# Kernel tuning notes

Hardware: AMD Instinct MI355X
Metric: run time of the kernel (lower is better)

The kernel has to match this reference:

```python
import jax, jax.numpy as jnp
import numpy as np

T_STEPS = 16
A = 64
B = 64
N = 16          # read_N
C = 3           # channels
H = 1024        # enc_size
IN = N * N * C  # LSTM input size = 768
EPS = 1e-8


def setup_inputs() -> dict:
    key = jax.random.key(0)
    ks = jax.random.split(key, 12)
    s = 0.02
    x = jax.random.normal(ks[0], (1024, C, B, A), dtype=jnp.float32)
    W_att = jax.random.normal(ks[1], (5, H), dtype=jnp.float32) * s
    b_att = jnp.zeros((5,), dtype=jnp.float32)
    W_ih = jax.random.normal(ks[2], (4 * H, IN), dtype=jnp.float32) * s
    W_hh = jax.random.normal(ks[3], (4 * H, H), dtype=jnp.float32) * s
    b_ih = jnp.zeros((4 * H,), dtype=jnp.float32)
    b_hh = jnp.zeros((4 * H,), dtype=jnp.float32)
    W_fc0 = jax.random.normal(ks[4], (H, H), dtype=jnp.float32) * s
    b_fc0 = jnp.zeros((H,), dtype=jnp.float32)
    W_fc = jax.random.normal(ks[5], (10, H), dtype=jnp.float32) * s
    b_fc = jnp.zeros((10,), dtype=jnp.float32)
    return {"x": x, "W_att": W_att, "b_att": b_att, "W_ih": W_ih, "W_hh": W_hh,
            "b_ih": b_ih, "b_hh": b_hh, "W_fc0": W_fc0, "b_fc0": b_fc0,
            "W_fc": W_fc, "b_fc": b_fc}


def _filterbank(gx, gy, sigma2, delta):
    # gx, gy, sigma2, delta: [Bt]
    grid = jnp.arange(N, dtype=jnp.float32)
    mu_x = gx[:, None] + (grid - N / 2 - 0.5) * delta[:, None]   # [Bt, N]
    mu_y = gy[:, None] + (grid - N / 2 - 0.5) * delta[:, None]   # [Bt, N]
    a = jnp.arange(A, dtype=jnp.float32)
    b = jnp.arange(B, dtype=jnp.float32)
    s2 = sigma2[:, None, None]
    Fx = jnp.exp(-(a[None, None, :] - mu_x[:, :, None]) ** 2 / (2 * s2))  # [Bt,N,A]
    Fy = jnp.exp(-(b[None, None, :] - mu_y[:, :, None]) ** 2 / (2 * s2))  # [Bt,N,B]
    Fx = Fx / (Fx.sum(2, keepdims=True) + EPS)
    Fy = Fy / (Fy.sum(2, keepdims=True) + EPS)
    return Fx, Fy


def _forward(x, W_att, b_att, W_ih, W_hh, b_ih, b_hh, W_fc0, b_fc0, W_fc, b_fc):
    Bt = x.shape[0]
    img = x.reshape(Bt, C, B, A)
    h0 = jnp.zeros((Bt, H), dtype=x.dtype)
    c0 = jnp.zeros((Bt, H), dtype=x.dtype)

    def step(carry, _):
        h, c = carry
        p = h @ W_att.T + b_att                      # [Bt, 5]
        gx_, gy_, log_s2, log_d, log_g = (p[:, 0], p[:, 1], p[:, 2], p[:, 3], p[:, 4])
        gx = (A + 1) / 2 * (gx_ + 1)
        gy = (B + 1) / 2 * (gy_ + 1)
        delta = (max(A, B) - 1) / (N - 1) * jnp.exp(log_d)
        sigma2 = jnp.exp(log_s2)
        gamma = jnp.exp(log_g)
        Fx, Fy = _filterbank(gx, gy, sigma2, delta)
        # glimpse[b,c] = Fy @ img[b,c] @ Fx^T -> [Bt, C, N, N]
        glimpse = jnp.einsum('bny,bcya,bxa->bcnx', Fy, img, Fx)
        r = glimpse.reshape(Bt, IN) * gamma[:, None]
        gates = r @ W_ih.T + b_ih + h @ W_hh.T + b_hh
        i_g, f_g, g_g, o_g = jnp.split(gates, 4, axis=1)
        c_new = jax.nn.sigmoid(f_g) * c + jax.nn.sigmoid(i_g) * jnp.tanh(g_g)
        h_new = jax.nn.sigmoid(o_g) * jnp.tanh(c_new)
        return (h_new, c_new), None

    (h, _), _ = jax.lax.scan(step, (h0, c0), None, length=T_STEPS)
    t = jax.nn.relu(h @ W_fc0.T + b_fc0)
    return t @ W_fc.T + b_fc


def reference(x, W_att, b_att, W_ih, W_hh, b_ih, b_hh, W_fc0, b_fc0, W_fc, b_fc):
    return _forward(x, W_att, b_att, W_ih, W_hh, b_ih, b_hh, W_fc0, b_fc0, W_fc, b_fc)
```

## Files before the change

kernel.cpp:

```cpp
#include <hip/hip_runtime.h>

typedef unsigned short u16;
typedef unsigned int u32;
typedef _Float16 f16;
typedef _Float16 half8 __attribute__((ext_vector_type(8)));
typedef _Float16 half4 __attribute__((ext_vector_type(4)));
typedef float f32x4 __attribute__((ext_vector_type(4)));

#define SPLIT_SC 2048.0f
#define SPLIT_INV (1.0f / 2048.0f)

__device__ __forceinline__ float sigf(float x) { return 1.0f / (1.0f + expf(-x)); }

__global__ __launch_bounds__(256) void att_glimpse(
    const f16* __restrict__ h_hi, const f16* __restrict__ h_lo,
    const float* __restrict__ Watt, const float* __restrict__ batt,
    const float* __restrict__ x,
    f16* __restrict__ r_hi, f16* __restrict__ r_lo)
{
    __shared__ float simg[64 * 64];
    __shared__ float sFx[16 * 68];
    __shared__ float sFyT[64 * 20];
    __shared__ float stmp[16 * 68];
    __shared__ float sred[4 * 5];
    __shared__ float spar[8];

    const int b = blockIdx.x, c = blockIdx.y, tid = threadIdx.x;
    const int lane = tid & 63, wave = tid >> 6;

    {
        const float4* src = (const float4*)(x + (size_t)b * 12288 + c * 4096);
        float4* dst = (float4*)simg;
        for (int i = tid; i < 1024; i += 256) dst[i] = src[i];
    }

    float p[5] = {0.f, 0.f, 0.f, 0.f, 0.f};
    {
        const f16* hh = h_hi + (size_t)b * 1024;
        const f16* hl = h_lo + (size_t)b * 1024;
        for (int k = tid; k < 1024; k += 256) {
            float hv = (float)hh[k] + (float)hl[k] * SPLIT_INV;
#pragma unroll
            for (int j = 0; j < 5; j++) p[j] += hv * Watt[j * 1024 + k];
        }
#pragma unroll
        for (int j = 0; j < 5; j++) {
#pragma unroll
            for (int o = 32; o > 0; o >>= 1) p[j] += __shfl_xor(p[j], o);
        }
        if (lane == 0) {
#pragma unroll
            for (int j = 0; j < 5; j++) sred[wave * 5 + j] = p[j];
        }
    }
    __syncthreads();
    if (tid == 0) {
        float q[5];
#pragma unroll
        for (int j = 0; j < 5; j++)
            q[j] = sred[j] + sred[5 + j] + sred[10 + j] + sred[15 + j] + batt[j];
        float q2 = fminf(fmaxf(q[2], -60.f), 60.f);
        float q3 = fminf(fmaxf(q[3], -60.f), 60.f);
        float q4 = fminf(fmaxf(q[4], -60.f), 60.f);
        spar[0] = 32.5f * (q[0] + 1.0f);
        spar[1] = 32.5f * (q[1] + 1.0f);
        spar[2] = 0.5f * expf(-q2);
        spar[3] = 4.2f * expf(q3);
        spar[4] = expf(q4);
    }
    __syncthreads();
    const float gx = spar[0], gy = spar[1], inv2s2 = spar[2], dl = spar[3],
                gamma = spar[4];

    {
        const float af = (float)lane;
#pragma unroll
        for (int i = 0; i < 4; i++) {
            int n = wave + i * 4;
            float nn = (float)n - 8.5f;
            float mux = gx + nn * dl;
            float ex = af - mux;
            float vx = expf(-ex * ex * inv2s2);
            float sx = vx;
#pragma unroll
            for (int o = 32; o > 0; o >>= 1) sx += __shfl_xor(sx, o);
            sFx[n * 68 + lane] = vx / (sx + 1e-8f);

            float muy = gy + nn * dl;
            float ey = af - muy;
            float vy = expf(-ey * ey * inv2s2);
            float sy = vy;
#pragma unroll
            for (int o = 32; o > 0; o >>= 1) sy += __shfl_xor(sy, o);
            sFyT[lane * 20 + n] = vy / (sy + 1e-8f);
        }
    }
    __syncthreads();

    if (wave == 0) {
        const int n4 = lane >> 4, a4 = lane & 15;
        f32x4 acc[4];
#pragma unroll
        for (int j = 0; j < 4; j++) acc[j] = (f32x4)(0.f);
        for (int y = 0; y < 64; y++) {
            float4 im = *(const float4*)(simg + y * 64 + a4 * 4);
            float4 fy = *(const float4*)(sFyT + y * 20 + n4 * 4);
            f32x4 iv = {im.x, im.y, im.z, im.w};
            acc[0] += fy.x * iv;
            acc[1] += fy.y * iv;
            acc[2] += fy.z * iv;
            acc[3] += fy.w * iv;
        }
#pragma unroll
        for (int j = 0; j < 4; j++)
            *(f32x4*)(stmp + (n4 * 4 + j) * 68 + a4 * 4) = acc[j];
    }
    __syncthreads();

    {
        const int n = tid >> 4, xo = tid & 15;
        const float* tp = stmp + n * 68;
        const float* fx = sFx + xo * 68;
        float s = 0.f;
        for (int a = 0; a < 64; a += 4) {
            float4 t4 = *(const float4*)(tp + a);
            float4 x4 = *(const float4*)(fx + a);
            s += t4.x * x4.x + t4.y * x4.y + t4.z * x4.z + t4.w * x4.w;
        }
        float v = s * gamma;
        f16 hi = (f16)v;
        size_t idx = (size_t)b * 768 + c * 256 + tid;
        r_hi[idx] = hi;
        r_lo[idx] = (f16)((v - (float)hi) * SPLIT_SC);
    }
}

__global__ __launch_bounds__(256) void swz_w(
    const float* __restrict__ W1, const float* __restrict__ W2,
    f16* __restrict__ out)
{
    const int kc = blockIdx.x >> 5, bn = blockIdx.x & 31;
    for (int t = threadIdx.x; t < 512; t += 256) {
        int c = t >> 6, lane = t & 63, l15 = lane & 15, lq = lane >> 4;
        int wrow = (c & 3) * 1024 + bn * 32 + l15 + ((c >> 2) << 4);
        const float* src;
        if (kc < 24) src = W1 + (size_t)wrow * 768 + kc * 32 + lq * 8;
        else         src = W2 + (size_t)wrow * 1024 + (kc - 24) * 32 + lq * 8;
        float4 g0 = *(const float4*)src;
        float4 g1 = *(const float4*)(src + 4);
        float gv[8] = {g0.x, g0.y, g0.z, g0.w, g1.x, g1.y, g1.z, g1.w};
        half8 hv, lv;
#pragma unroll
        for (int j = 0; j < 8; j++) {
            f16 h = (f16)gv[j];
            hv[j] = h;
            lv[j] = (f16)((gv[j] - (float)h) * SPLIT_SC);
        }
        size_t base = ((size_t)(kc * 32 + bn) * 16 + c * 2) * 512 + (size_t)lane * 8;
        *(half8*)(out + base) = hv;
        *(half8*)(out + base + 512) = lv;
    }
}

#define LDH 40

__global__ __launch_bounds__(256, 2) void gates_lstm(
    const f16* __restrict__ A1h, const f16* __restrict__ A1l,
    const f16* __restrict__ A2h, const f16* __restrict__ A2l,
    const f16* __restrict__ Wswz,
    const float* __restrict__ b1, const float* __restrict__ b2,
    float* __restrict__ cst,
    f16* __restrict__ Hh, f16* __restrict__ Hl)
{
    __shared__ f16 sA[2][2][64 * LDH];
    const int tid = threadIdx.x;
    const int kb = blockIdx.x;
    const int xcd = kb & 7, jb = kb >> 3;
    const int bn = xcd * 4 + (jb & 3);
    const int bm = jb >> 2;
    const int wave = tid >> 6, lane = tid & 63;
    const int wm = (wave >> 1) * 32;
    const int cbase = (wave & 1) * 4;
    const int l15 = lane & 15, lq = lane >> 4;
    const int arow = tid >> 2, acol = (tid & 3) * 8;

    f32x4 ah[2][4], al[2][4];
#pragma unroll
    for (int i = 0; i < 2; i++)
#pragma unroll
        for (int j = 0; j < 4; j++) { ah[i][j] = (f32x4)(0.f); al[i][j] = (f32x4)(0.f); }

    {
        size_t aoff = (size_t)(bm * 64 + arow) * 768 + acol;
        *(uint4*)&sA[0][0][arow * LDH + acol] = *(const uint4*)(A1h + aoff);
        *(uint4*)&sA[0][1][arow * LDH + acol] = *(const uint4*)(A1l + aoff);
    }
    half8 Bc[8];
    {
        const f16* wb = Wswz + (size_t)bn * 16 * 512 + (size_t)lane * 8;
#pragma unroll
        for (int nt = 0; nt < 4; nt++) {
            Bc[nt * 2]     = *(const half8*)(wb + (cbase + nt) * 1024);
            Bc[nt * 2 + 1] = *(const half8*)(wb + (cbase + nt) * 1024 + 512);
        }
    }

#pragma unroll 2
    for (int i = 0; i < 56; ++i) {
        const int cur = i & 1;
        __syncthreads();
        const int kn = (i + 1 < 56) ? i + 1 : 55;
        const f16 *pah, *pal; int astr, ako;
        if (kn < 24) { pah = A1h; pal = A1l; astr = 768;  ako = kn * 32; }
        else         { pah = A2h; pal = A2l; astr = 1024; ako = (kn - 24) * 32; }
        size_t aoff = (size_t)(bm * 64 + arow) * astr + ako + acol;
        uint4 vh = *(const uint4*)(pah + aoff);
        uint4 vl = *(const uint4*)(pal + aoff);
        half8 Bn[8];
        {
            const f16* wb = Wswz + (size_t)(kn * 32 + bn) * 16 * 512 + (size_t)lane * 8;
#pragma unroll
            for (int nt = 0; nt < 4; nt++) {
                Bn[nt * 2]     = *(const half8*)(wb + (cbase + nt) * 1024);
                Bn[nt * 2 + 1] = *(const half8*)(wb + (cbase + nt) * 1024 + 512);
            }
        }
        half8 afh[2], afl[2];
#pragma unroll
        for (int mt = 0; mt < 2; mt++) {
            int ro = (wm + mt * 16 + l15) * LDH + lq * 8;
            afh[mt] = *(const half8*)&sA[cur][0][ro];
            afl[mt] = *(const half8*)&sA[cur][1][ro];
        }
#pragma unroll
        for (int mt = 0; mt < 2; mt++)
#pragma unroll
            for (int nt = 0; nt < 4; nt++) {
                ah[mt][nt] = __builtin_amdgcn_mfma_f32_16x16x32_f16(
                    afh[mt], Bc[nt * 2], ah[mt][nt], 0, 0, 0);
                al[mt][nt] = __builtin_amdgcn_mfma_f32_16x16x32_f16(
                    afh[mt], Bc[nt * 2 + 1], al[mt][nt], 0, 0, 0);
                al[mt][nt] = __builtin_amdgcn_mfma_f32_16x16x32_f16(
                    afl[mt], Bc[nt * 2], al[mt][nt], 0, 0, 0);
            }
        const int nxt = cur ^ 1;
        *(uint4*)&sA[nxt][0][arow * LDH + acol] = vh;
        *(uint4*)&sA[nxt][1][arow * LDH + acol] = vl;
#pragma unroll
        for (int q = 0; q < 8; q++) Bc[q] = Bn[q];
    }

    const int u = bn * 32 + l15 + ((wave & 1) << 4);
    float bvs[4];
#pragma unroll
    for (int g = 0; g < 4; g++) bvs[g] = b1[g * 1024 + u] + b2[g * 1024 + u];
#pragma unroll
    for (int mt = 0; mt < 2; mt++) {
#pragma unroll
        for (int rg = 0; rg < 4; rg++) {
            int row = bm * 64 + wm + mt * 16 + lq * 4 + rg;
            size_t idx = (size_t)row * 1024 + u;
            float gi = ah[mt][0][rg] + al[mt][0][rg] * SPLIT_INV + bvs[0];
            float gf = ah[mt][1][rg] + al[mt][1][rg] * SPLIT_INV + bvs[1];
            float gg = ah[mt][2][rg] + al[mt][2][rg] * SPLIT_INV + bvs[2];
            float go = ah[mt][3][rg] + al[mt][3][rg] * SPLIT_INV + bvs[3];
            float cn = sigf(gf) * cst[idx] + sigf(gi) * tanhf(gg);
            float hn = sigf(go) * tanhf(cn);
            cst[idx] = cn;
            f16 hh = (f16)hn;
            Hh[idx] = hh;
            Hl[idx] = (f16)((hn - (float)hh) * SPLIT_SC);
        }
    }
}

__global__ __launch_bounds__(256, 1) void fc0_gemm(
    const f16* __restrict__ Ah, const f16* __restrict__ Al,
    const float* __restrict__ W, const float* __restrict__ bias,
    float* __restrict__ out)
{
    __shared__ f16 sAh[128 * LDH], sAl[128 * LDH];
    __shared__ f16 sBh[128 * LDH], sBl[128 * LDH];
    const int tid = threadIdx.x;
    const int bm = blockIdx.x, bn = blockIdx.y;
    const int wave = tid >> 6, lane = tid & 63;
    const int wm = (wave >> 1) * 64, wn = (wave & 1) * 64;
    const int l15 = lane & 15, lq = lane >> 4;

    f32x4 ach[4][4], acx[4][4];
#pragma unroll
    for (int i = 0; i < 4; i++)
#pragma unroll
        for (int j = 0; j < 4; j++) { ach[i][j] = (f32x4)(0.f); acx[i][j] = (f32x4)(0.f); }

    for (int kc = 0; kc < 1024; kc += 32) {
#pragma unroll
        for (int l = 0; l < 2; l++) {
            int e = (l * 256 + tid) * 8;
            int row = e >> 5, col = e & 31;
            size_t off = (size_t)(bm * 128 + row) * 1024 + kc + col;
            *(uint4*)&sAh[row * LDH + col] = *(const uint4*)(Ah + off);
            *(uint4*)&sAl[row * LDH + col] = *(const uint4*)(Al + off);
        }
#pragma unroll
        for (int l = 0; l < 4; l++) {
            int e = (l * 256 + tid) * 4;
            int crow = e >> 5, col = e & 31;
            float4 g = *(const float4*)(W + (size_t)(bn * 128 + crow) * 1024 + kc + col);
            f16 h0 = (f16)g.x, h1 = (f16)g.y, h2 = (f16)g.z, h3 = (f16)g.w;
            half4 hv = {h0, h1, h2, h3};
            half4 lv = {(f16)((g.x - (float)h0) * SPLIT_SC),
                        (f16)((g.y - (float)h1) * SPLIT_SC),
                        (f16)((g.z - (float)h2) * SPLIT_SC),
                        (f16)((g.w - (float)h3) * SPLIT_SC)};
            *(half4*)&sBh[crow * LDH + col] = hv;
            *(half4*)&sBl[crow * LDH + col] = lv;
        }
        __syncthreads();
        half8 afh[4], afl[4], bfh[4], bfl[4];
#pragma unroll
        for (int mt = 0; mt < 4; mt++) {
            int ro = (wm + mt * 16 + l15) * LDH + lq * 8;
            afh[mt] = *(const half8*)&sAh[ro];
            afl[mt] = *(const half8*)&sAl[ro];
        }
#pragma unroll
        for (int nt = 0; nt < 4; nt++) {
            int ro = (wn + nt * 16 + l15) * LDH + lq * 8;
            bfh[nt] = *(const half8*)&sBh[ro];
            bfl[nt] = *(const half8*)&sBl[ro];
        }
#pragma unroll
        for (int mt = 0; mt < 4; mt++)
#pragma unroll
            for (int nt = 0; nt < 4; nt++) {
                ach[mt][nt] = __builtin_amdgcn_mfma_f32_16x16x32_f16(
                    afh[mt], bfh[nt], ach[mt][nt], 0, 0, 0);
                acx[mt][nt] = __builtin_amdgcn_mfma_f32_16x16x32_f16(
                    afh[mt], bfl[nt], acx[mt][nt], 0, 0, 0);
                acx[mt][nt] = __builtin_amdgcn_mfma_f32_16x16x32_f16(
                    afl[mt], bfh[nt], acx[mt][nt], 0, 0, 0);
            }
        __syncthreads();
    }

#pragma unroll
    for (int mt = 0; mt < 4; mt++) {
#pragma unroll
        for (int nt = 0; nt < 4; nt++) {
            int col = bn * 128 + wn + nt * 16 + l15;
            float bv = bias[col];
#pragma unroll
            for (int rg = 0; rg < 4; rg++) {
                int row = bm * 128 + wm + mt * 16 + lq * 4 + rg;
                float v = ach[mt][nt][rg] + acx[mt][nt][rg] * SPLIT_INV + bv;
                out[(size_t)row * 1024 + col] = fmaxf(v, 0.f);
            }
        }
    }
}

__global__ __launch_bounds__(64) void fc_out(
    const float* __restrict__ tb, const float* __restrict__ Wfc,
    const float* __restrict__ bfc, float* __restrict__ out)
{
    int b = blockIdx.x, lane = threadIdx.x;
    const float* tv = tb + (size_t)b * 1024;
    float p[10];
#pragma unroll
    for (int j = 0; j < 10; j++) p[j] = 0.f;
    for (int k = lane; k < 1024; k += 64) {
        float t = tv[k];
#pragma unroll
        for (int j = 0; j < 10; j++) p[j] += t * Wfc[j * 1024 + k];
    }
#pragma unroll
    for (int j = 0; j < 10; j++) {
#pragma unroll
        for (int o = 32; o > 0; o >>= 1) p[j] += __shfl_xor(p[j], o);
    }
    if (lane == 0) {
#pragma unroll
        for (int j = 0; j < 10; j++) out[b * 10 + j] = p[j] + bfc[j];
    }
}

extern "C" void kernel_launch(void* const* d_in, const int* in_sizes, int n_in,
                              void* d_out, int out_size, void* d_ws, size_t ws_size,
                              hipStream_t stream)
{
    const float* x     = (const float*)d_in[0];
    const float* W_att = (const float*)d_in[1];
    const float* b_att = (const float*)d_in[2];
    const float* W_ih  = (const float*)d_in[3];
    const float* W_hh  = (const float*)d_in[4];
    const float* b_ih  = (const float*)d_in[5];
    const float* b_hh  = (const float*)d_in[6];
    const float* W_fc0 = (const float*)d_in[7];
    const float* b_fc0 = (const float*)d_in[8];
    const float* W_fc  = (const float*)d_in[9];
    const float* b_fc  = (const float*)d_in[10];
    float* out = (float*)d_out;

    char* ws = (char*)d_ws;
    f16*   Wswz   = (f16*)ws;    ws += (size_t)56 * 32 * 16 * 512 * 2;
    float* c_f32  = (float*)ws;  ws += (size_t)1024 * 1024 * 4;
    f16*   h_hi0  = (f16*)ws;    ws += (size_t)1024 * 1024 * 2;
    f16*   h_hi1  = (f16*)ws;    ws += (size_t)1024 * 1024 * 2;
    f16*   h_lo0  = (f16*)ws;    ws += (size_t)1024 * 1024 * 2;
    f16*   h_lo1  = (f16*)ws;    ws += (size_t)1024 * 1024 * 2;
    f16*   r_hi   = (f16*)ws;    ws += (size_t)1024 * 768 * 2;
    f16*   r_lo   = (f16*)ws;    ws += (size_t)1024 * 768 * 2;
    float* t_f32  = c_f32;
    f16* h_hi[2] = {h_hi0, h_hi1};
    f16* h_lo[2] = {h_lo0, h_lo1};

    hipMemsetAsync(c_f32, 0, (size_t)1024 * 1024 * 4, stream);
    hipMemsetAsync(h_hi0, 0, (size_t)1024 * 1024 * 2, stream);
    hipMemsetAsync(h_lo0, 0, (size_t)1024 * 1024 * 2, stream);

    swz_w<<<56 * 32, 256, 0, stream>>>(W_ih, W_hh, Wswz);

    for (int t = 0; t < 16; t++) {
        int rb = t & 1, wb = 1 - rb;
        att_glimpse<<<dim3(1024, 3), 256, 0, stream>>>(
            h_hi[rb], h_lo[rb], W_att, b_att, x, r_hi, r_lo);
        gates_lstm<<<512, 256, 0, stream>>>(
            r_hi, r_lo, h_hi[rb], h_lo[rb], Wswz, b_ih, b_hh,
            c_f32, h_hi[wb], h_lo[wb]);
    }
    fc0_gemm<<<dim3(8, 8), 256, 0, stream>>>(
        h_hi[0], h_lo[0], W_fc0, b_fc0, t_f32);
    fc_out<<<1024, 64, 0, stream>>>(t_f32, W_fc, b_fc, out);
}
```

Before: 1.523 ms.

## Store activations in MFMA fragment layout and drop LDS staging in GEMMs

Hidden state and glimpse vectors are now written directly in a pre-swizzled MFMA fragment layout, with hi and lo halves interleaved. This lets gates_lstm and fc0_gemm load A fragments straight from global memory with no LDS staging or barriers. gates_lstm moves to 128-row tiles with 256 blocks, so each wave computes a 64x32 tile, and fc0's weights are pre-swizzled by a new kernel. The costs are scattered 2-byte stores in att_glimpse and the LSTM epilogue, no software prefetch of the next K chunk, and fewer, larger blocks that may lower occupancy.

```diff
diff --git a/kernel.cpp b/kernel.cpp
--- a/kernel.cpp
+++ b/kernel.cpp
@@ -12,11 +12,16 @@
 
 __device__ __forceinline__ float sigf(float x) { return 1.0f / (1.0f + expf(-x)); }
 
+__device__ __forceinline__ size_t frag_addr(int row, int k) {
+    return ((size_t)((k >> 5) * 64 + (row >> 4)) * 2) * 512
+         + (size_t)((((k & 31) >> 3) << 4) + (row & 15)) * 8 + (k & 7);
+}
+
 __global__ __launch_bounds__(256) void att_glimpse(
-    const f16* __restrict__ h_hi, const f16* __restrict__ h_lo,
+    const f16* __restrict__ hs,
     const float* __restrict__ Watt, const float* __restrict__ batt,
     const float* __restrict__ x,
-    f16* __restrict__ r_hi, f16* __restrict__ r_lo)
+    f16* __restrict__ r_swz)
 {
     __shared__ float simg[64 * 64];
     __shared__ float sFx[16 * 68];
@@ -36,10 +41,9 @@
 
     float p[5] = {0.f, 0.f, 0.f, 0.f, 0.f};
     {
-        const f16* hh = h_hi + (size_t)b * 1024;
-        const f16* hl = h_lo + (size_t)b * 1024;
         for (int k = tid; k < 1024; k += 256) {
-            float hv = (float)hh[k] + (float)hl[k] * SPLIT_INV;
+            size_t ba = frag_addr(b, k);
+            float hv = (float)hs[ba] + (float)hs[ba + 512] * SPLIT_INV;
 #pragma unroll
             for (int j = 0; j < 5; j++) p[j] += hv * Watt[j * 1024 + k];
         }
@@ -129,9 +133,10 @@
         }
         float v = s * gamma;
         f16 hi = (f16)v;
-        size_t idx = (size_t)b * 768 + c * 256 + tid;
-        r_hi[idx] = hi;
-        r_lo[idx] = (f16)((v - (float)hi) * SPLIT_SC);
+        int k = c * 256 + tid;
+        size_t ba = frag_addr(b, k);
+        r_swz[ba] = hi;
+        r_swz[ba + 512] = (f16)((v - (float)hi) * SPLIT_SC);
     }
 }
 
@@ -162,103 +167,95 @@
     }
 }
 
-#define LDH 40
-
-__global__ __launch_bounds__(256, 2) void gates_lstm(
-    const f16* __restrict__ A1h, const f16* __restrict__ A1l,
-    const f16* __restrict__ A2h, const f16* __restrict__ A2l,
+__global__ __launch_bounds__(256) void swz_wfc(
+    const float* __restrict__ W, f16* __restrict__ out)
+{
+    const int kc = blockIdx.x >> 4, cn = blockIdx.x & 15;
+    const int ct = threadIdx.x >> 6, lane = threadIdx.x & 63;
+    const int l15 = lane & 15, lq = lane >> 4;
+    int wrow = cn * 64 + ct * 16 + l15;
+    const float* src = W + (size_t)wrow * 1024 + kc * 32 + lq * 8;
+    float4 g0 = *(const float4*)src;
+    float4 g1 = *(const float4*)(src + 4);
+    float gv[8] = {g0.x, g0.y, g0.z, g0.w, g1.x, g1.y, g1.z, g1.w};
+    half8 hv, lv;
+#pragma unroll
+    for (int j = 0; j < 8; j++) {
+        f16 h = (f16)gv[j];
+        hv[j] = h;
+        lv[j] = (f16)((gv[j] - (float)h) * SPLIT_SC);
+    }
+    size_t base = ((size_t)(kc * 16 + cn) * 8 + ct * 2) * 512 + (size_t)lane * 8;
+    *(half8*)(out + base) = hv;
+    *(half8*)(out + base + 512) = lv;
+}
+
+__global__ __launch_bounds__(256, 1) void gates_lstm(
+    const f16* __restrict__ r_swz,
+    const f16* __restrict__ h_swz,
     const f16* __restrict__ Wswz,
     const float* __restrict__ b1, const float* __restrict__ b2,
     float* __restrict__ cst,
-    f16* __restrict__ Hh, f16* __restrict__ Hl)
-{
-    __shared__ f16 sA[2][2][64 * LDH];
+    f16* __restrict__ Hout)
+{
     const int tid = threadIdx.x;
     const int kb = blockIdx.x;
     const int xcd = kb & 7, jb = kb >> 3;
     const int bn = xcd * 4 + (jb & 3);
     const int bm = jb >> 2;
     const int wave = tid >> 6, lane = tid & 63;
-    const int wm = (wave >> 1) * 32;
-    const int cbase = (wave & 1) * 4;
+    const int wrow = wave >> 1;
+    const int wcol = wave & 1;
     const int l15 = lane & 15, lq = lane >> 4;
-    const int arow = tid >> 2, acol = (tid & 3) * 8;
-
-    f32x4 ah[2][4], al[2][4];
-#pragma unroll
-    for (int i = 0; i < 2; i++)
+    const int rtb = bm * 8 + wrow * 4;
+
+    f32x4 ah[4][4], al[4][4];
+#pragma unroll
+    for (int i = 0; i < 4; i++)
 #pragma unroll
         for (int j = 0; j < 4; j++) { ah[i][j] = (f32x4)(0.f); al[i][j] = (f32x4)(0.f); }
 
-    {
-        size_t aoff = (size_t)(bm * 64 + arow) * 768 + acol;
-        *(uint4*)&sA[0][0][arow * LDH + acol] = *(const uint4*)(A1h + aoff);
-        *(uint4*)&sA[0][1][arow * LDH + acol] = *(const uint4*)(A1l + aoff);
-    }
-    half8 Bc[8];
-    {
-        const f16* wb = Wswz + (size_t)bn * 16 * 512 + (size_t)lane * 8;
+#pragma unroll 2
+    for (int kc = 0; kc < 56; ++kc) {
+        const f16* Ab; size_t ak;
+        if (kc < 24) { Ab = r_swz; ak = (size_t)kc * 64; }
+        else         { Ab = h_swz; ak = (size_t)(kc - 24) * 64; }
+        half8 afh[4], afl[4], bfh[4], bfl[4];
+#pragma unroll
+        for (int mt = 0; mt < 4; mt++) {
+            const f16* p = Ab + ((ak + rtb + mt) * 2) * 512 + lane * 8;
+            afh[mt] = *(const half8*)p;
+            afl[mt] = *(const half8*)(p + 512);
+        }
+        const f16* wb = Wswz + ((size_t)(kc * 32 + bn) * 16 + wcol * 8) * 512
+                      + (size_t)lane * 8;
 #pragma unroll
         for (int nt = 0; nt < 4; nt++) {
-            Bc[nt * 2]     = *(const half8*)(wb + (cbase + nt) * 1024);
-            Bc[nt * 2 + 1] = *(const half8*)(wb + (cbase + nt) * 1024 + 512);
-        }
-    }
-
-#pragma unroll 2
-    for (int i = 0; i < 56; ++i) {
-        const int cur = i & 1;
-        __syncthreads();
-        const int kn = (i + 1 < 56) ? i + 1 : 55;
-        const f16 *pah, *pal; int astr, ako;
-        if (kn < 24) { pah = A1h; pal = A1l; astr = 768;  ako = kn * 32; }
-        else         { pah = A2h; pal = A2l; astr = 1024; ako = (kn - 24) * 32; }
-        size_t aoff = (size_t)(bm * 64 + arow) * astr + ako + acol;
-        uint4 vh = *(const uint4*)(pah + aoff);
-        uint4 vl = *(const uint4*)(pal + aoff);
-        half8 Bn[8];
-        {
-            const f16* wb = Wswz + (size_t)(kn * 32 + bn) * 16 * 512 + (size_t)lane * 8;
-#pragma unroll
-            for (int nt = 0; nt < 4; nt++) {
-                Bn[nt * 2]     = *(const half8*)(wb + (cbase + nt) * 1024);
-                Bn[nt * 2 + 1] = *(const half8*)(wb + (cbase + nt) * 1024 + 512);
-            }
-        }
-        half8 afh[2], afl[2];
-#pragma unroll
-        for (int mt = 0; mt < 2; mt++) {
-            int ro = (wm + mt * 16 + l15) * LDH + lq * 8;
-            afh[mt] = *(const half8*)&sA[cur][0][ro];
-            afl[mt] = *(const half8*)&sA[cur][1][ro];
-        }
-#pragma unroll
-        for (int mt = 0; mt < 2; mt++)
+            bfh[nt] = *(const half8*)(wb + nt * 1024);
+            bfl[nt] = *(const half8*)(wb + nt * 1024 + 512);
+        }
+#pragma unroll
+        for (int mt = 0; mt < 4; mt++)
 #pragma unroll
             for (int nt = 0; nt < 4; nt++) {
                 ah[mt][nt] = __builtin_amdgcn_mfma_f32_16x16x32_f16(
-                    afh[mt], Bc[nt * 2], ah[mt][nt], 0, 0, 0);
+                    afh[mt], bfh[nt], ah[mt][nt], 0, 0, 0);
                 al[mt][nt] = __builtin_amdgcn_mfma_f32_16x16x32_f16(
-                    afh[mt], Bc[nt * 2 + 1], al[mt][nt], 0, 0, 0);
+                    afh[mt], bfl[nt], al[mt][nt], 0, 0, 0);
                 al[mt][nt] = __builtin_amdgcn_mfma_f32_16x16x32_f16(
-                    afl[mt], Bc[nt * 2], al[mt][nt], 0, 0, 0);
+                    afl[mt], bfh[nt], al[mt][nt], 0, 0, 0);
             }
-        const int nxt = cur ^ 1;
-        *(uint4*)&sA[nxt][0][arow * LDH + acol] = vh;
-        *(uint4*)&sA[nxt][1][arow * LDH + acol] = vl;
-#pragma unroll
-        for (int q = 0; q < 8; q++) Bc[q] = Bn[q];
-    }
-
-    const int u = bn * 32 + l15 + ((wave & 1) << 4);
+    }
+
+    const int u = bn * 32 + l15 + (wcol << 4);
     float bvs[4];
 #pragma unroll
     for (int g = 0; g < 4; g++) bvs[g] = b1[g * 1024 + u] + b2[g * 1024 + u];
 #pragma unroll
-    for (int mt = 0; mt < 2; mt++) {
+    for (int mt = 0; mt < 4; mt++) {
 #pragma unroll
         for (int rg = 0; rg < 4; rg++) {
-            int row = bm * 64 + wm + mt * 16 + lq * 4 + rg;
+            int row = bm * 128 + wrow * 64 + mt * 16 + lq * 4 + rg;
             size_t idx = (size_t)row * 1024 + u;
             float gi = ah[mt][0][rg] + al[mt][0][rg] * SPLIT_INV + bvs[0];
             float gf = ah[mt][1][rg] + al[mt][1][rg] * SPLIT_INV + bvs[1];
@@ -268,94 +265,57 @@
             float hn = sigf(go) * tanhf(cn);
             cst[idx] = cn;
             f16 hh = (f16)hn;
-            Hh[idx] = hh;
-            Hl[idx] = (f16)((hn - (float)hh) * SPLIT_SC);
+            size_t ba = frag_addr(row, u);
+            Hout[ba] = hh;
+            Hout[ba + 512] = (f16)((hn - (float)hh) * SPLIT_SC);
         }
     }
 }
 
 __global__ __launch_bounds__(256, 1) void fc0_gemm(
-    const f16* __restrict__ Ah, const f16* __restrict__ Al,
-    const float* __restrict__ W, const float* __restrict__ bias,
-    float* __restrict__ out)
-{
-    __shared__ f16 sAh[128 * LDH], sAl[128 * LDH];
-    __shared__ f16 sBh[128 * LDH], sBl[128 * LDH];
+    const f16* __restrict__ h_swz, const f16* __restrict__ Wf,
+    const float* __restrict__ bias, float* __restrict__ out)
+{
     const int tid = threadIdx.x;
-    const int bm = blockIdx.x, bn = blockIdx.y;
+    const int bm = blockIdx.x >> 4, cn = blockIdx.x & 15;
     const int wave = tid >> 6, lane = tid & 63;
-    const int wm = (wave >> 1) * 64, wn = (wave & 1) * 64;
     const int l15 = lane & 15, lq = lane >> 4;
 
-    f32x4 ach[4][4], acx[4][4];
-#pragma unroll
-    for (int i = 0; i < 4; i++)
-#pragma unroll
-        for (int j = 0; j < 4; j++) { ach[i][j] = (f32x4)(0.f); acx[i][j] = (f32x4)(0.f); }
-
-    for (int kc = 0; kc < 1024; kc += 32) {
-#pragma unroll
-        for (int l = 0; l < 2; l++) {
-            int e = (l * 256 + tid) * 8;
-            int row = e >> 5, col = e & 31;
-            size_t off = (size_t)(bm * 128 + row) * 1024 + kc + col;
-            *(uint4*)&sAh[row * LDH + col] = *(const uint4*)(Ah + off);
-            *(uint4*)&sAl[row * LDH + col] = *(const uint4*)(Al + off);
-        }
-#pragma unroll
-        for (int l = 0; l < 4; l++) {
-            int e = (l * 256 + tid) * 4;
-            int crow = e >> 5, col = e & 31;
-            float4 g = *(const float4*)(W + (size_t)(bn * 128 + crow) * 1024 + kc + col);
-            f16 h0 = (f16)g.x, h1 = (f16)g.y, h2 = (f16)g.z, h3 = (f16)g.w;
-            half4 hv = {h0, h1, h2, h3};
-            half4 lv = {(f16)((g.x - (float)h0) * SPLIT_SC),
-                        (f16)((g.y - (float)h1) * SPLIT_SC),
-                        (f16)((g.z - (float)h2) * SPLIT_SC),
-                        (f16)((g.w - (float)h3) * SPLIT_SC)};
-            *(half4*)&sBh[crow * LDH + col] = hv;
-            *(half4*)&sBl[crow * LDH + col] = lv;
-        }
-        __syncthreads();
-        half8 afh[4], afl[4], bfh[4], bfl[4];
+    f32x4 ah[4], al[4];
+#pragma unroll
+    for (int i = 0; i < 4; i++) { ah[i] = (f32x4)(0.f); al[i] = (f32x4)(0.f); }
+
+#pragma unroll 2
+    for (int kc = 0; kc < 32; ++kc) {
+        half8 afh[4], afl[4];
 #pragma unroll
         for (int mt = 0; mt < 4; mt++) {
-            int ro = (wm + mt * 16 + l15) * LDH + lq * 8;
-            afh[mt] = *(const half8*)&sAh[ro];
-            afl[mt] = *(const half8*)&sAl[ro];
-        }
-#pragma unroll
-        for (int nt = 0; nt < 4; nt++) {
-            int ro = (wn + nt * 16 + l15) * LDH + lq * 8;
-            bfh[nt] = *(const half8*)&sBh[ro];
-            bfl[nt] = *(const half8*)&sBl[ro];
-        }
-#pragma unroll
-        for (int mt = 0; mt < 4; mt++)
-#pragma unroll
-            for (int nt = 0; nt < 4; nt++) {
-                ach[mt][nt] = __builtin_amdgcn_mfma_f32_16x16x32_f16(
-                    afh[mt], bfh[nt], ach[mt][nt], 0, 0, 0);
-                acx[mt][nt] = __builtin_amdgcn_mfma_f32_16x16x32_f16(
-                    afh[mt], bfl[nt], acx[mt][nt], 0, 0, 0);
-                acx[mt][nt] = __builtin_amdgcn_mfma_f32_16x16x32_f16(
-                    afl[mt], bfh[nt], acx[mt][nt], 0, 0, 0);
-            }
-        __syncthreads();
-    }
-
+            const f16* p = h_swz + ((size_t)(kc * 64 + bm * 4 + mt) * 2) * 512
+                         + (size_t)lane * 8;
+            afh[mt] = *(const half8*)p;
+            afl[mt] = *(const half8*)(p + 512);
+        }
+        const f16* wb = Wf + ((size_t)(kc * 16 + cn) * 8 + wave * 2) * 512
+                      + (size_t)lane * 8;
+        half8 bfh = *(const half8*)wb;
+        half8 bfl = *(const half8*)(wb + 512);
+#pragma unroll
+        for (int mt = 0; mt < 4; mt++) {
+            ah[mt] = __builtin_amdgcn_mfma_f32_16x16x32_f16(afh[mt], bfh, ah[mt], 0, 0, 0);
+            al[mt] = __builtin_amdgcn_mfma_f32_16x16x32_f16(afh[mt], bfl, al[mt], 0, 0, 0);
+            al[mt] = __builtin_amdgcn_mfma_f32_16x16x32_f16(afl[mt], bfh, al[mt], 0, 0, 0);
+        }
+    }
+
+    const int col = cn * 64 + wave * 16 + l15;
+    const float bv = bias[col];
 #pragma unroll
     for (int mt = 0; mt < 4; mt++) {
 #pragma unroll
-        for (int nt = 0; nt < 4; nt++) {
-            int col = bn * 128 + wn + nt * 16 + l15;
-            float bv = bias[col];
-#pragma unroll
-            for (int rg = 0; rg < 4; rg++) {
-                int row = bm * 128 + wm + mt * 16 + lq * 4 + rg;
-                float v = ach[mt][nt][rg] + acx[mt][nt][rg] * SPLIT_INV + bv;
-                out[(size_t)row * 1024 + col] = fmaxf(v, 0.f);
-            }
+        for (int rg = 0; rg < 4; rg++) {
+            int row = bm * 64 + mt * 16 + lq * 4 + rg;
+            float v = ah[mt][rg] + al[mt][rg] * SPLIT_INV + bv;
+            out[(size_t)row * 1024 + col] = fmaxf(v, 0.f);
         }
     }
 }
@@ -404,32 +364,27 @@
 
     char* ws = (char*)d_ws;
     f16*   Wswz   = (f16*)ws;    ws += (size_t)56 * 32 * 16 * 512 * 2;
+    f16*   Wfcswz = (f16*)ws;    ws += (size_t)32 * 16 * 8 * 512 * 2;
     float* c_f32  = (float*)ws;  ws += (size_t)1024 * 1024 * 4;
-    f16*   h_hi0  = (f16*)ws;    ws += (size_t)1024 * 1024 * 2;
-    f16*   h_hi1  = (f16*)ws;    ws += (size_t)1024 * 1024 * 2;
-    f16*   h_lo0  = (f16*)ws;    ws += (size_t)1024 * 1024 * 2;
-    f16*   h_lo1  = (f16*)ws;    ws += (size_t)1024 * 1024 * 2;
-    f16*   r_hi   = (f16*)ws;    ws += (size_t)1024 * 768 * 2;
-    f16*   r_lo   = (f16*)ws;    ws += (size_t)1024 * 768 * 2;
+    f16*   h_swz0 = (f16*)ws;    ws += (size_t)32 * 64 * 2 * 512 * 2;
+    f16*   h_swz1 = (f16*)ws;    ws += (size_t)32 * 64 * 2 * 512 * 2;
+    f16*   r_swz  = (f16*)ws;    ws += (size_t)24 * 64 * 2 * 512 * 2;
     float* t_f32  = c_f32;
-    f16* h_hi[2] = {h_hi0, h_hi1};
-    f16* h_lo[2] = {h_lo0, h_lo1};
+    f16* h_swz[2] = {h_swz0, h_swz1};
 
     hipMemsetAsync(c_f32, 0, (size_t)1024 * 1024 * 4, stream);
-    hipMemsetAsync(h_hi0, 0, (size_t)1024 * 1024 * 2, stream);
-    hipMemsetAsync(h_lo0, 0, (size_t)1024 * 1024 * 2, stream);
+    hipMemsetAsync(h_swz0, 0, (size_t)32 * 64 * 2 * 512 * 2, stream);
 
     swz_w<<<56 * 32, 256, 0, stream>>>(W_ih, W_hh, Wswz);
+    swz_wfc<<<32 * 16, 256, 0, stream>>>(W_fc0, Wfcswz);
 
     for (int t = 0; t < 16; t++) {
         int rb = t & 1, wb = 1 - rb;
         att_glimpse<<<dim3(1024, 3), 256, 0, stream>>>(
-            h_hi[rb], h_lo[rb], W_att, b_att, x, r_hi, r_lo);
-        gates_lstm<<<512, 256, 0, stream>>>(
-            r_hi, r_lo, h_hi[rb], h_lo[rb], Wswz, b_ih, b_hh,
-            c_f32, h_hi[wb], h_lo[wb]);
-    }
-    fc0_gemm<<<dim3(8, 8), 256, 0, stream>>>(
-        h_hi[0], h_lo[0], W_fc0, b_fc0, t_f32);
+            h_swz[rb], W_att, b_att, x, r_swz);
+        gates_lstm<<<256, 256, 0, stream>>>(
+            r_swz, h_swz[rb], Wswz, b_ih, b_hh, c_f32, h_swz[wb]);
+    }
+    fc0_gemm<<<256, 256, 0, stream>>>(h_swz[0], Wfcswz, b_fc0, t_f32);
     fc_out<<<1024, 64, 0, stream>>>(t_f32, W_fc, b_fc, out);
 }
```

Measured after the change: 1.988 ms. +30.5%, slower.
